# Kernel tuning notes

Measured on AMD Instinct MI355X. Metric: run time of the kernel, lower is better.

Reference implementation:

```python
import jax, jax.numpy as jnp
import numpy as np

BUCKETS = 32
DIM = 1024
HEADS = 16
TEMP = 0.75
SINK_ITERS = 7
LOG_EPS = 1e-6
GUMBEL_EPS = 1e-4


def _sinkhorn(r, n_iters):
    # iterative row/col log-normalization, then exp (matches torch loop)
    for _ in range(n_iters):
        r = r - jax.scipy.special.logsumexp(r, axis=2, keepdims=True)
        r = r - jax.scipy.special.logsumexp(r, axis=1, keepdims=True)
    return jnp.exp(r)


def setup_inputs() -> dict:
    key = jax.random.key(0)
    kq, kk, kv, kw, kg = jax.random.split(key, 5)
    B, H, T, DH = 4, 16, 4096, 64
    q = jax.random.normal(kq, (B, H, T, DH), jnp.float32)
    k = jax.random.normal(kk, (B, H, T, DH), jnp.float32)
    v = jax.random.normal(kv, (B, H, T, DH), jnp.float32)
    sort_w = jax.random.normal(kw, (1, H, DH, BUCKETS), jnp.float32)
    u = jax.random.uniform(kg, (B * H, BUCKETS, BUCKETS), jnp.float32, 0.0, 1.0)
    gumbel_noise = -jnp.log(-jnp.log(u + GUMBEL_EPS) + GUMBEL_EPS)
    return {"q": q, "k": k, "v": v, "sort_w": sort_w, "gumbel_noise": gumbel_noise}


def reference(q, k, v, sort_w, gumbel_noise):
    b, h, t, dh = q.shape
    bh = b * h
    bsz = t // BUCKETS  # tokens per bucket
    # bucket: (bh, buckets, bsz, dh)
    qb = q.reshape(bh, BUCKETS, bsz, dh)
    kb = k.reshape(bh, BUCKETS, bsz, dh)
    vb = v.reshape(bh, BUCKETS, bsz, dh)
    # bucket summaries for routing
    b_k_r = kb.sum(axis=2)  # (bh, buckets, dh)
    e_w = jnp.broadcast_to(sort_w, (b, h, dh, BUCKETS)).reshape(bh, dh, BUCKETS)
    R = jnp.log(jax.nn.relu(jnp.einsum('bud,bdv->buv', b_k_r, e_w)) + LOG_EPS)
    R = (R + gumbel_noise) / TEMP
    R = _sinkhorn(R, SINK_ITERS)  # soft permutation matrix (bh, buckets, buckets)
    R = jnp.tril(R, -1)  # causal: only attend to strictly earlier buckets
    # soft-permute key/value buckets
    k_re = jnp.einsum('buv,bvtd->butd', R, kb)
    v_re = jnp.einsum('buv,bvtd->butd', R, vb)
    bk = jnp.concatenate([k_re, kb], axis=2)  # (bh, buckets, 2*bsz, dh)
    bv = jnp.concatenate([v_re, vb], axis=2)
    dots = jnp.einsum('buie,buje->buij', qb, bk) * (DIM ** -0.5)
    attn = jax.nn.softmax(dots, axis=-1)
    out = jnp.einsum('buij,buje->buie', attn, bv)  # (bh, buckets, bsz, dh)
    return out.reshape(b, h, t, dh)
```

## Files before the change

### kernel.cpp

```cpp
#include <hip/hip_runtime.h>
#include <hip/hip_bf16.h>

#define BUCKETS 32
#define BSZ 128
#define DH 64
#define TEMPINV 1.3333333333333333f
#define SINK_ITERS 7
#define LOG_EPS 1e-6f
#define SCALE 0.03125f

typedef short bf16x8 __attribute__((ext_vector_type(8)));
typedef float f32x4 __attribute__((ext_vector_type(4)));

__device__ __forceinline__ void bf8_to_f32(const uint4 x, float* f) {
    f[0] = __uint_as_float(x.x << 16);
    f[1] = __uint_as_float(x.x & 0xffff0000u);
    f[2] = __uint_as_float(x.y << 16);
    f[3] = __uint_as_float(x.y & 0xffff0000u);
    f[4] = __uint_as_float(x.z << 16);
    f[5] = __uint_as_float(x.z & 0xffff0000u);
    f[6] = __uint_as_float(x.w << 16);
    f[7] = __uint_as_float(x.w & 0xffff0000u);
}

__device__ __forceinline__ unsigned f2bf(float f) {
    unsigned x = __float_as_uint(f);
    return (x + 0x7fffu + ((x >> 16) & 1u)) >> 16;
}

__device__ __forceinline__ uint4 packbf8(const float* f) {
    uint4 r;
    r.x = f2bf(f[0]) | (f2bf(f[1]) << 16);
    r.y = f2bf(f[2]) | (f2bf(f[3]) << 16);
    r.z = f2bf(f[4]) | (f2bf(f[5]) << 16);
    r.w = f2bf(f[6]) | (f2bf(f[7]) << 16);
    return r;
}

__device__ __forceinline__ void load_lds16(const uint4* g, uint4* l) {
    __builtin_amdgcn_global_load_lds(
        (const __attribute__((address_space(1))) unsigned int*)g,
        (__attribute__((address_space(3))) unsigned int*)l, 16, 0, 0);
}

__global__ __launch_bounds__(256) void bksum_kernel(
    const float* __restrict__ kptr, float* __restrict__ bkr)
{
    const int t = blockIdx.x;
    const int tid = threadIdx.x;
    __shared__ float4 part[16][17];
    const float4* k4 = (const float4*)kptr + (size_t)t * 2048;
    const int c4 = tid & 15, rg = tid >> 4;
    float4 s; s.x = 0.f; s.y = 0.f; s.z = 0.f; s.w = 0.f;
    for (int r = rg; r < 128; r += 16) {
        float4 a = k4[r * 16 + c4];
        s.x += a.x; s.y += a.y; s.z += a.z; s.w += a.w;
    }
    part[rg][c4] = s;
    __syncthreads();
    if (tid < 16) {
        float4 acc = part[0][tid];
        for (int g = 1; g < 16; ++g) {
            float4 p = part[g][tid];
            acc.x += p.x; acc.y += p.y; acc.z += p.z; acc.w += p.w;
        }
        ((float4*)bkr)[t * 16 + tid] = acc;
    }
}

__global__ __launch_bounds__(256) void sinkhorn_kernel(
    const float* __restrict__ bkrp,
    const float* __restrict__ swptr,
    const float* __restrict__ gptr,
    float* __restrict__ Rout)
{
    const int b = blockIdx.x;
    const int h = b & 15;
    const int tid = threadIdx.x;

    __shared__ float bk[BUCKETS][DH];
    __shared__ float sw[DH][BUCKETS];
    __shared__ float R[BUCKETS][BUCKETS + 1];

    for (int o = tid; o < DH * BUCKETS; o += 256)
        sw[o >> 5][o & 31] = swptr[h * DH * BUCKETS + o];
    for (int o = tid; o < BUCKETS * DH; o += 256)
        bk[o >> 6][o & 63] = bkrp[b * 2048 + o];
    __syncthreads();

    for (int o = tid; o < BUCKETS * BUCKETS; o += 256) {
        const int uu = o >> 5, vv = o & 31;
        float dot = 0.f;
        for (int d = 0; d < DH; ++d) dot = fmaf(bk[uu][d], sw[d][vv], dot);
        const float g = gptr[b * 1024 + o];
        R[uu][vv] = (logf(fmaxf(dot, 0.f) + LOG_EPS) + g) * TEMPINV;
    }
    __syncthreads();

    for (int it = 0; it < SINK_ITERS; ++it) {
        if (tid < BUCKETS) {
            float m = -1e30f;
            for (int j = 0; j < BUCKETS; ++j) m = fmaxf(m, R[tid][j]);
            float s = 0.f;
            for (int j = 0; j < BUCKETS; ++j) s += expf(R[tid][j] - m);
            const float lse = m + logf(s);
            for (int j = 0; j < BUCKETS; ++j) R[tid][j] -= lse;
        }
        __syncthreads();
        if (tid < BUCKETS) {
            float m = -1e30f;
            for (int j = 0; j < BUCKETS; ++j) m = fmaxf(m, R[j][tid]);
            float s = 0.f;
            for (int j = 0; j < BUCKETS; ++j) s += expf(R[j][tid] - m);
            const float lse = m + logf(s);
            for (int j = 0; j < BUCKETS; ++j) R[j][tid] -= lse;
        }
        __syncthreads();
    }

    for (int o = tid; o < BUCKETS * BUCKETS; o += 256) {
        const int uu = o >> 5, vv = o & 31;
        Rout[b * 1024 + o] = (vv < uu) ? expf(R[uu][vv]) : 0.f;
    }
}

__global__ __launch_bounds__(256) void reshuffle2_kernel(
    const float* __restrict__ kptr,
    const float* __restrict__ vptr,
    const float* __restrict__ Rmat,
    uint4* __restrict__ kimg,
    uint4* __restrict__ vimg)
{
    const int j0 = blockIdx.x;
    const int b  = blockIdx.y;
    const int tid = threadIdx.x;
    const int u = tid >> 3, c8 = tid & 7;

    __shared__ float ls[32][8][64];
    __shared__ float lr[32][33];

    for (int o = tid; o < 1024; o += 256)
        lr[o >> 5][o & 31] = Rmat[b * 1024 + o];

    float4* ls4 = (float4*)ls;

    {
        const float4* kb4 = (const float4*)kptr + (size_t)b * 65536 + j0 * 128;
        for (int it = 0; it < 16; ++it) {
            const int idx = it * 256 + tid;
            const int v = idx >> 7, i = idx & 127;
            ls4[v * 128 + i] = kb4[v * 2048 + i];
        }
    }
    __syncthreads();
    {
        float ka[8][8];
        #pragma unroll
        for (int r = 0; r < 8; ++r)
            #pragma unroll
            for (int t = 0; t < 8; ++t) ka[r][t] = 0.f;
        for (int vv = 0; vv < u; ++vv) {
            const float rw = lr[u][vv];
            #pragma unroll
            for (int r = 0; r < 8; ++r)
                #pragma unroll
                for (int t = 0; t < 8; ++t)
                    ka[r][t] = fmaf(rw, ls[vv][r][c8 * 8 + t], ka[r][t]);
        }
        uint4* kdst = kimg + ((size_t)b * 32 + u) * 2048;
        #pragma unroll
        for (int r = 0; r < 8; ++r) {
            kdst[(j0 * 8 + r) * 8 + (c8 ^ r)] = packbf8(ka[r]);
            float o8[8];
            #pragma unroll
            for (int t = 0; t < 8; ++t) o8[t] = ls[u][r][c8 * 8 + t];
            kdst[(128 + j0 * 8 + r) * 8 + (c8 ^ r)] = packbf8(o8);
        }
    }
    __syncthreads();

    {
        const float4* vb4 = (const float4*)vptr + (size_t)b * 65536 + j0 * 128;
        for (int it = 0; it < 16; ++it) {
            const int idx = it * 256 + tid;
            const int v = idx >> 7, i = idx & 127;
            ls4[v * 128 + i] = vb4[v * 2048 + i];
        }
    }
    __syncthreads();
    {
        float va[8][8];
        #pragma unroll
        for (int r = 0; r < 8; ++r)
            #pragma unroll
            for (int t = 0; t < 8; ++t) va[r][t] = 0.f;
        for (int vv = 0; vv < u; ++vv) {
            const float rw = lr[u][vv];
            #pragma unroll
            for (int r = 0; r < 8; ++r)
                #pragma unroll
                for (int t = 0; t < 8; ++t)
                    va[r][t] = fmaf(rw, ls[vv][r][c8 * 8 + t], va[r][t]);
        }
        uint4* vdst = vimg + ((size_t)b * 32 + u) * 2048;
        #pragma unroll
        for (int t = 0; t < 8; ++t) {
            const int blk = c8 * 8 + (t ^ c8);
            uint4 wre;
            wre.x = f2bf(va[0][t]) | (f2bf(va[1][t]) << 16);
            wre.y = f2bf(va[2][t]) | (f2bf(va[3][t]) << 16);
            wre.z = f2bf(va[4][t]) | (f2bf(va[5][t]) << 16);
            wre.w = f2bf(va[6][t]) | (f2bf(va[7][t]) << 16);
            vdst[j0 * 64 + blk] = wre;
            uint4 wor;
            wor.x = f2bf(ls[u][0][c8 * 8 + t]) | (f2bf(ls[u][1][c8 * 8 + t]) << 16);
            wor.y = f2bf(ls[u][2][c8 * 8 + t]) | (f2bf(ls[u][3][c8 * 8 + t]) << 16);
            wor.z = f2bf(ls[u][4][c8 * 8 + t]) | (f2bf(ls[u][5][c8 * 8 + t]) << 16);
            wor.w = f2bf(ls[u][6][c8 * 8 + t]) | (f2bf(ls[u][7][c8 * 8 + t]) << 16);
            vdst[(16 + j0) * 64 + blk] = wor;
        }
    }
}

__global__ __launch_bounds__(128) void attn_fallback(
    const float* __restrict__ qptr,
    const float* __restrict__ kptr,
    const float* __restrict__ vptr,
    const float* __restrict__ Rmat,
    float4* __restrict__ optr)
{
    const int u = blockIdx.x;
    const int b = blockIdx.y;
    const int tid = threadIdx.x;

    __shared__ uint4 sbk[2048];
    __shared__ uint4 sbv[2048];

    const float4* k4 = (const float4*)kptr + (size_t)b * 65536;
    const float4* v4 = (const float4*)vptr + (size_t)b * 65536;
    const float4* q4 = (const float4*)qptr + (size_t)b * 65536;

    const float* Rrow = Rmat + (b * BUCKETS + u) * BUCKETS;
    for (int o = tid; o < 1024; o += 128) {
        float ka[8] = {0.f,0.f,0.f,0.f,0.f,0.f,0.f,0.f};
        float va[8] = {0.f,0.f,0.f,0.f,0.f,0.f,0.f,0.f};
        for (int vv = 0; vv < u; ++vv) {
            const float r = Rrow[vv];
            float4 a = k4[vv * 2048 + 2 * o], c = k4[vv * 2048 + 2 * o + 1];
            ka[0] = fmaf(r, a.x, ka[0]); ka[1] = fmaf(r, a.y, ka[1]);
            ka[2] = fmaf(r, a.z, ka[2]); ka[3] = fmaf(r, a.w, ka[3]);
            ka[4] = fmaf(r, c.x, ka[4]); ka[5] = fmaf(r, c.y, ka[5]);
            ka[6] = fmaf(r, c.z, ka[6]); ka[7] = fmaf(r, c.w, ka[7]);
            float4 av = v4[vv * 2048 + 2 * o], cv = v4[vv * 2048 + 2 * o + 1];
            va[0] = fmaf(r, av.x, va[0]); va[1] = fmaf(r, av.y, va[1]);
            va[2] = fmaf(r, av.z, va[2]); va[3] = fmaf(r, av.w, va[3]);
            va[4] = fmaf(r, cv.x, va[4]); va[5] = fmaf(r, cv.y, va[5]);
            va[6] = fmaf(r, cv.z, va[6]); va[7] = fmaf(r, cv.w, va[7]);
        }
        sbk[o] = packbf8(ka);
        sbv[o] = packbf8(va);
        float4 a = k4[u * 2048 + 2 * o], c = k4[u * 2048 + 2 * o + 1];
        float f[8] = {a.x,a.y,a.z,a.w,c.x,c.y,c.z,c.w};
        sbk[1024 + o] = packbf8(f);
        float4 av = v4[u * 2048 + 2 * o], cv = v4[u * 2048 + 2 * o + 1];
        float g[8] = {av.x,av.y,av.z,av.w,cv.x,cv.y,cv.z,cv.w};
        sbv[1024 + o] = packbf8(g);
    }
    __syncthreads();

    const int i = tid;
    float qr[64];
    const float4* qrow = q4 + (u * 128 + i) * 16;
    for (int d4 = 0; d4 < 16; ++d4) {
        float4 t = qrow[d4];
        qr[d4 * 4 + 0] = t.x; qr[d4 * 4 + 1] = t.y;
        qr[d4 * 4 + 2] = t.z; qr[d4 * 4 + 3] = t.w;
    }

    float acc[64];
    for (int d = 0; d < 64; ++d) acc[d] = 0.f;
    float l = 0.f;

    for (int j = 0; j < 256; ++j) {
        float s = 0.f;
        for (int d8 = 0; d8 < 8; ++d8) {
            float f[8];
            bf8_to_f32(sbk[j * 8 + d8], f);
            for (int t = 0; t < 8; ++t) s = fmaf(qr[d8 * 8 + t], f[t], s);
        }
        const float p = __expf(s * SCALE);
        l += p;
        for (int d8 = 0; d8 < 8; ++d8) {
            float f[8];
            bf8_to_f32(sbv[j * 8 + d8], f);
            for (int t = 0; t < 8; ++t)
                acc[d8 * 8 + t] = fmaf(p, f[t], acc[d8 * 8 + t]);
        }
    }

    const float inv = 1.f / l;
    float4* orow = optr + (size_t)b * 65536 + (u * 128 + i) * 16;
    for (int d4 = 0; d4 < 16; ++d4) {
        float4 t;
        t.x = acc[d4 * 4 + 0] * inv;
        t.y = acc[d4 * 4 + 1] * inv;
        t.z = acc[d4 * 4 + 2] * inv;
        t.w = acc[d4 * 4 + 3] * inv;
        orow[d4] = t;
    }
}

__global__ __launch_bounds__(256) void attn_mfma2(
    const float* __restrict__ qptr,
    const uint4* __restrict__ kimg,
    const uint4* __restrict__ vimg,
    float* __restrict__ optr)
{
    const int u = blockIdx.x;
    const int b = blockIdx.y;
    const int tid = threadIdx.x;
    const int lane = tid & 63;
    const int w = tid >> 6;
    const int lg = lane >> 4;
    const int lr = lane & 15;

    __shared__ uint4 sK[2048];
    __shared__ uint4 sV[2048];
    __shared__ uint4 sP[1024];

    const size_t tile = (size_t)b * 32 + u;
    const uint4* gk = kimg + tile * 2048;
    const uint4* gv = vimg + tile * 2048;

    #pragma unroll
    for (int it = 0; it < 8; ++it)
        load_lds16(gk + it * 256 + tid, &sK[it * 256 + (w << 6)]);
    #pragma unroll
    for (int it = 0; it < 8; ++it)
        load_lds16(gv + it * 256 + tid, &sV[it * 256 + (w << 6)]);

    const float* qbase = qptr + (size_t)b * 262144 + (size_t)u * 8192;
    bf16x8 qf[2][2];
    #pragma unroll
    for (int mt = 0; mt < 2; ++mt)
        #pragma unroll
        for (int c = 0; c < 2; ++c) {
            const int row = w * 32 + mt * 16 + lr;
            const float4* qr = (const float4*)(qbase + row * 64 + (c * 4 + lg) * 8);
            float4 a = qr[0], cc = qr[1];
            float f[8] = {a.x * SCALE, a.y * SCALE, a.z * SCALE, a.w * SCALE,
                          cc.x * SCALE, cc.y * SCALE, cc.z * SCALE, cc.w * SCALE};
            uint4 tq = packbf8(f);
            qf[mt][c] = *(bf16x8*)&tq;
        }
    __syncthreads();

    uint4* sPw = sP + w * 256;
    unsigned short* sPh = (unsigned short*)sPw;

    f32x4 acc[2][4];
    float lsum[2][4];
    #pragma unroll
    for (int mt = 0; mt < 2; ++mt) {
        #pragma unroll
        for (int nt = 0; nt < 4; ++nt) {
            acc[mt][nt][0] = 0.f; acc[mt][nt][1] = 0.f;
            acc[mt][nt][2] = 0.f; acc[mt][nt][3] = 0.f;
        }
        #pragma unroll
        for (int r = 0; r < 4; ++r) lsum[mt][r] = 0.f;
    }

    for (int kb = 0; kb < 4; ++kb) {
        bf16x8 kf[4][2];
        #pragma unroll
        for (int nt = 0; nt < 4; ++nt)
            #pragma unroll
            for (int c = 0; c < 2; ++c) {
                const int j = kb * 64 + nt * 16 + lr;
                const int dcu = c * 4 + lg;
                uint4 t = sK[j * 8 + (dcu ^ (j & 7))];
                kf[nt][c] = *(bf16x8*)&t;
            }
        f32x4 s[2][4];
        #pragma unroll
        for (int mt = 0; mt < 2; ++mt)
            #pragma unroll
            for (int nt = 0; nt < 4; ++nt) {
                s[mt][nt][0] = 0.f; s[mt][nt][1] = 0.f;
                s[mt][nt][2] = 0.f; s[mt][nt][3] = 0.f;
            }
        __builtin_amdgcn_s_setprio(1);
        #pragma unroll
        for (int c = 0; c < 2; ++c)
            #pragma unroll
            for (int mt = 0; mt < 2; ++mt)
                #pragma unroll
                for (int nt = 0; nt < 4; ++nt)
                    s[mt][nt] = __builtin_amdgcn_mfma_f32_16x16x32_bf16(
                        qf[mt][c], kf[nt][c], s[mt][nt], 0, 0, 0);
        __builtin_amdgcn_s_setprio(0);

        #pragma unroll
        for (int mt = 0; mt < 2; ++mt)
            #pragma unroll
            for (int nt = 0; nt < 4; ++nt)
                #pragma unroll
                for (int r = 0; r < 4; ++r) {
                    const float p = __expf(s[mt][nt][r]);
                    lsum[mt][r] += p;
                    const int row = mt * 16 + lg * 4 + r;
                    const int col = nt * 16 + lr;
                    sPh[row * 64 + (((col >> 3) ^ (row & 7)) << 3) + (col & 7)] =
                        (unsigned short)f2bf(p);
                }
        asm volatile("s_waitcnt lgkmcnt(0)" ::: "memory");
        __builtin_amdgcn_sched_barrier(0);

        bf16x8 pf[2][2];
        #pragma unroll
        for (int mt = 0; mt < 2; ++mt)
            #pragma unroll
            for (int c = 0; c < 2; ++c) {
                const int row = mt * 16 + lr;
                const int dcu = c * 4 + lg;
                uint4 t = sPw[row * 8 + (dcu ^ (row & 7))];
                pf[mt][c] = *(bf16x8*)&t;
            }
        bf16x8 vf[4][2];
        #pragma unroll
        for (int nt = 0; nt < 4; ++nt)
            #pragma unroll
            for (int c = 0; c < 2; ++c) {
                const int p = kb * 8 + c * 4 + lg;
                const int d = nt * 16 + lr;
                const int blk = (d >> 3) * 8 + ((d & 7) ^ ((d >> 3) & 7));
                uint4 t = sV[p * 64 + blk];
                vf[nt][c] = *(bf16x8*)&t;
            }
        __builtin_amdgcn_s_setprio(1);
        #pragma unroll
        for (int c = 0; c < 2; ++c)
            #pragma unroll
            for (int mt = 0; mt < 2; ++mt)
                #pragma unroll
                for (int nt = 0; nt < 4; ++nt)
                    acc[mt][nt] = __builtin_amdgcn_mfma_f32_16x16x32_bf16(
                        pf[mt][c], vf[nt][c], acc[mt][nt], 0, 0, 0);
        __builtin_amdgcn_s_setprio(0);
    }

    #pragma unroll
    for (int mt = 0; mt < 2; ++mt)
        #pragma unroll
        for (int r = 0; r < 4; ++r) {
            float sum = lsum[mt][r];
            sum += __shfl_xor(sum, 1);
            sum += __shfl_xor(sum, 2);
            sum += __shfl_xor(sum, 4);
            sum += __shfl_xor(sum, 8);
            const float inv = 1.f / sum;
            const int row = mt * 16 + lg * 4 + r;
            float* orow = optr + (size_t)b * 262144 +
                          (size_t)(u * 128 + w * 32 + row) * 64;
            #pragma unroll
            for (int nt = 0; nt < 4; ++nt)
                orow[nt * 16 + lr] = acc[mt][nt][r] * inv;
        }
}

extern "C" void kernel_launch(void* const* d_in, const int* in_sizes, int n_in,
                              void* d_out, int out_size, void* d_ws, size_t ws_size,
                              hipStream_t stream) {
    const float* q  = (const float*)d_in[0];
    const float* k  = (const float*)d_in[1];
    const float* v  = (const float*)d_in[2];
    const float* sw = (const float*)d_in[3];
    const float* g  = (const float*)d_in[4];

    float* R    = (float*)d_ws;
    float* bkr  = (float*)((char*)d_ws + 262144);
    uint4* kimg = (uint4*)((char*)d_ws + 1048576);
    uint4* vimg = (uint4*)((char*)d_ws + 1048576 + 67108864);
    const bool big_ws = (ws_size >= (size_t)1048576 + 2u * 67108864u);

    bksum_kernel<<<dim3(2048), dim3(256), 0, stream>>>(k, bkr);
    sinkhorn_kernel<<<dim3(64), dim3(256), 0, stream>>>(bkr, sw, g, R);
    if (big_ws) {
        reshuffle2_kernel<<<dim3(16, 64), dim3(256), 0, stream>>>(k, v, R, kimg, vimg);
        attn_mfma2<<<dim3(32, 64), dim3(256), 0, stream>>>(q, kimg, vimg, (float*)d_out);
    } else {
        attn_fallback<<<dim3(32, 64), dim3(128), 0, stream>>>(q, k, v, R, (float4*)d_out);
    }
}
```

Baseline: 328.8 us.

## Fuse sinkhorn into reshuffle kernel, parallelize LSE, halve reshuffle tile

Drops the separate sinkhorn launch on the main path: each reshuffle block now recomputes the routing logits and runs the Sinkhorn normalization itself, and the row and column logsumexp uses 256 threads with shuffle reductions instead of 32 serial threads. Each reshuffle block now handles 4 token rows instead of 8, doubling the grid to 32x64 and halving shared memory, with launch bounds set for higher occupancy. The cost is that the routing and Sinkhorn work is repeated 32 times per head-batch, and V writes become 8-byte half stores.

Result: slower. 340.4 us (+3.5%).

```diff
diff --git a/kernel.cpp b/kernel.cpp
--- a/kernel.cpp
+++ b/kernel.cpp
@@ -97,25 +97,36 @@
     }
     __syncthreads();
 
+    const int rr = tid >> 3, sub = tid & 7;
     for (int it = 0; it < SINK_ITERS; ++it) {
-        if (tid < BUCKETS) {
-            float m = -1e30f;
-            for (int j = 0; j < BUCKETS; ++j) m = fmaxf(m, R[tid][j]);
-            float s = 0.f;
-            for (int j = 0; j < BUCKETS; ++j) s += expf(R[tid][j] - m);
+        {
+            float vals[4];
+            float m = -1e30f, s = 0.f;
+            #pragma unroll
+            for (int q = 0; q < 4; ++q) { vals[q] = R[rr][sub * 4 + q]; m = fmaxf(m, vals[q]); }
+            m = fmaxf(m, __shfl_xor(m, 1)); m = fmaxf(m, __shfl_xor(m, 2)); m = fmaxf(m, __shfl_xor(m, 4));
+            #pragma unroll
+            for (int q = 0; q < 4; ++q) s += expf(vals[q] - m);
+            s += __shfl_xor(s, 1); s += __shfl_xor(s, 2); s += __shfl_xor(s, 4);
             const float lse = m + logf(s);
-            for (int j = 0; j < BUCKETS; ++j) R[tid][j] -= lse;
-        }
-        __syncthreads();
-        if (tid < BUCKETS) {
-            float m = -1e30f;
-            for (int j = 0; j < BUCKETS; ++j) m = fmaxf(m, R[j][tid]);
-            float s = 0.f;
-            for (int j = 0; j < BUCKETS; ++j) s += expf(R[j][tid] - m);
+            #pragma unroll
+            for (int q = 0; q < 4; ++q) R[rr][sub * 4 + q] = vals[q] - lse;
+            __syncthreads();
+        }
+        {
+            float vals[4];
+            float m = -1e30f, s = 0.f;
+            #pragma unroll
+            for (int q = 0; q < 4; ++q) { vals[q] = R[sub * 4 + q][rr]; m = fmaxf(m, vals[q]); }
+            m = fmaxf(m, __shfl_xor(m, 1)); m = fmaxf(m, __shfl_xor(m, 2)); m = fmaxf(m, __shfl_xor(m, 4));
+            #pragma unroll
+            for (int q = 0; q < 4; ++q) s += expf(vals[q] - m);
+            s += __shfl_xor(s, 1); s += __shfl_xor(s, 2); s += __shfl_xor(s, 4);
             const float lse = m + logf(s);
-            for (int j = 0; j < BUCKETS; ++j) R[j][tid] -= lse;
-        }
-        __syncthreads();
+            #pragma unroll
+            for (int q = 0; q < 4; ++q) R[sub * 4 + q][rr] = vals[q] - lse;
+            __syncthreads();
+        }
     }
 
     for (int o = tid; o < BUCKETS * BUCKETS; o += 256) {
@@ -124,100 +135,150 @@
     }
 }
 
-__global__ __launch_bounds__(256) void reshuffle2_kernel(
+__global__ __launch_bounds__(256, 4) void reshuffle3_kernel(
     const float* __restrict__ kptr,
     const float* __restrict__ vptr,
-    const float* __restrict__ Rmat,
+    const float* __restrict__ bkrp,
+    const float* __restrict__ swptr,
+    const float* __restrict__ gptr,
     uint4* __restrict__ kimg,
     uint4* __restrict__ vimg)
 {
     const int j0 = blockIdx.x;
     const int b  = blockIdx.y;
+    const int h  = b & 15;
     const int tid = threadIdx.x;
     const int u = tid >> 3, c8 = tid & 7;
 
-    __shared__ float ls[32][8][64];
+    __shared__ float ls[32][4][64];
     __shared__ float lr[32][33];
 
-    for (int o = tid; o < 1024; o += 256)
-        lr[o >> 5][o & 31] = Rmat[b * 1024 + o];
+    float* bk  = &ls[0][0][0];
+    float* swl = bk + 2048;
+
+    for (int o = tid; o < 2048; o += 256) bk[o]  = bkrp[b * 2048 + o];
+    for (int o = tid; o < 2048; o += 256) swl[o] = swptr[h * 2048 + o];
+    __syncthreads();
+    for (int o = tid; o < 1024; o += 256) {
+        const int uu = o >> 5, vv = o & 31;
+        float dot = 0.f;
+        for (int d = 0; d < 64; ++d) dot = fmaf(bk[uu * 64 + d], swl[d * 32 + vv], dot);
+        lr[uu][vv] = (logf(fmaxf(dot, 0.f) + LOG_EPS) + gptr[b * 1024 + o]) * TEMPINV;
+    }
+    __syncthreads();
+
+    const int rr = tid >> 3, sub = tid & 7;
+    for (int it = 0; it < SINK_ITERS; ++it) {
+        {
+            float vals[4];
+            float m = -1e30f, s = 0.f;
+            #pragma unroll
+            for (int q = 0; q < 4; ++q) { vals[q] = lr[rr][sub * 4 + q]; m = fmaxf(m, vals[q]); }
+            m = fmaxf(m, __shfl_xor(m, 1)); m = fmaxf(m, __shfl_xor(m, 2)); m = fmaxf(m, __shfl_xor(m, 4));
+            #pragma unroll
+            for (int q = 0; q < 4; ++q) s += expf(vals[q] - m);
+            s += __shfl_xor(s, 1); s += __shfl_xor(s, 2); s += __shfl_xor(s, 4);
+            const float lse = m + logf(s);
+            #pragma unroll
+            for (int q = 0; q < 4; ++q) lr[rr][sub * 4 + q] = vals[q] - lse;
+            __syncthreads();
+        }
+        {
+            float vals[4];
+            float m = -1e30f, s = 0.f;
+            #pragma unroll
+            for (int q = 0; q < 4; ++q) { vals[q] = lr[sub * 4 + q][rr]; m = fmaxf(m, vals[q]); }
+            m = fmaxf(m, __shfl_xor(m, 1)); m = fmaxf(m, __shfl_xor(m, 2)); m = fmaxf(m, __shfl_xor(m, 4));
+            #pragma unroll
+            for (int q = 0; q < 4; ++q) s += expf(vals[q] - m);
+            s += __shfl_xor(s, 1); s += __shfl_xor(s, 2); s += __shfl_xor(s, 4);
+            const float lse = m + logf(s);
+            #pragma unroll
+            for (int q = 0; q < 4; ++q) lr[sub * 4 + q][rr] = vals[q] - lse;
+            __syncthreads();
+        }
+    }
+    for (int o = tid; o < 1024; o += 256) {
+        const int uu = o >> 5, vv = o & 31;
+        const float val = lr[uu][vv];
+        lr[uu][vv] = (vv < uu) ? expf(val) : 0.f;
+    }
+    __syncthreads();
 
     float4* ls4 = (float4*)ls;
 
     {
-        const float4* kb4 = (const float4*)kptr + (size_t)b * 65536 + j0 * 128;
-        for (int it = 0; it < 16; ++it) {
+        const float4* kb4 = (const float4*)kptr + (size_t)b * 65536 + j0 * 64;
+        for (int it = 0; it < 8; ++it) {
             const int idx = it * 256 + tid;
-            const int v = idx >> 7, i = idx & 127;
-            ls4[v * 128 + i] = kb4[v * 2048 + i];
+            const int v = idx >> 6, i = idx & 63;
+            ls4[v * 64 + i] = kb4[v * 2048 + i];
         }
     }
     __syncthreads();
     {
-        float ka[8][8];
-        #pragma unroll
-        for (int r = 0; r < 8; ++r)
+        float ka[4][8];
+        #pragma unroll
+        for (int r = 0; r < 4; ++r)
             #pragma unroll
             for (int t = 0; t < 8; ++t) ka[r][t] = 0.f;
         for (int vv = 0; vv < u; ++vv) {
-            const float rw = lr[u][vv];
-            #pragma unroll
-            for (int r = 0; r < 8; ++r)
+            const float rwt = lr[u][vv];
+            #pragma unroll
+            for (int r = 0; r < 4; ++r)
                 #pragma unroll
                 for (int t = 0; t < 8; ++t)
-                    ka[r][t] = fmaf(rw, ls[vv][r][c8 * 8 + t], ka[r][t]);
+                    ka[r][t] = fmaf(rwt, ls[vv][r][c8 * 8 + t], ka[r][t]);
         }
         uint4* kdst = kimg + ((size_t)b * 32 + u) * 2048;
         #pragma unroll
-        for (int r = 0; r < 8; ++r) {
-            kdst[(j0 * 8 + r) * 8 + (c8 ^ r)] = packbf8(ka[r]);
+        for (int r = 0; r < 4; ++r) {
+            const int j = j0 * 4 + r;
+            kdst[j * 8 + (c8 ^ (j & 7))] = packbf8(ka[r]);
             float o8[8];
             #pragma unroll
             for (int t = 0; t < 8; ++t) o8[t] = ls[u][r][c8 * 8 + t];
-            kdst[(128 + j0 * 8 + r) * 8 + (c8 ^ r)] = packbf8(o8);
+            kdst[(128 + j) * 8 + (c8 ^ (j & 7))] = packbf8(o8);
         }
     }
     __syncthreads();
 
     {
-        const float4* vb4 = (const float4*)vptr + (size_t)b * 65536 + j0 * 128;
-        for (int it = 0; it < 16; ++it) {
+        const float4* vb4 = (const float4*)vptr + (size_t)b * 65536 + j0 * 64;
+        for (int it = 0; it < 8; ++it) {
             const int idx = it * 256 + tid;
-            const int v = idx >> 7, i = idx & 127;
-            ls4[v * 128 + i] = vb4[v * 2048 + i];
+            const int v = idx >> 6, i = idx & 63;
+            ls4[v * 64 + i] = vb4[v * 2048 + i];
         }
     }
     __syncthreads();
     {
-        float va[8][8];
-        #pragma unroll
-        for (int r = 0; r < 8; ++r)
+        float va[4][8];
+        #pragma unroll
+        for (int r = 0; r < 4; ++r)
             #pragma unroll
             for (int t = 0; t < 8; ++t) va[r][t] = 0.f;
         for (int vv = 0; vv < u; ++vv) {
-            const float rw = lr[u][vv];
-            #pragma unroll
-            for (int r = 0; r < 8; ++r)
+            const float rwt = lr[u][vv];
+            #pragma unroll
+            for (int r = 0; r < 4; ++r)
                 #pragma unroll
                 for (int t = 0; t < 8; ++t)
-                    va[r][t] = fmaf(rw, ls[vv][r][c8 * 8 + t], va[r][t]);
-        }
-        uint4* vdst = vimg + ((size_t)b * 32 + u) * 2048;
+                    va[r][t] = fmaf(rwt, ls[vv][r][c8 * 8 + t], va[r][t]);
+        }
+        uint2* vdst2 = (uint2*)(vimg + ((size_t)b * 32 + u) * 2048);
+        const int p = j0 >> 1, half = j0 & 1;
         #pragma unroll
         for (int t = 0; t < 8; ++t) {
             const int blk = c8 * 8 + (t ^ c8);
-            uint4 wre;
+            uint2 wre;
             wre.x = f2bf(va[0][t]) | (f2bf(va[1][t]) << 16);
             wre.y = f2bf(va[2][t]) | (f2bf(va[3][t]) << 16);
-            wre.z = f2bf(va[4][t]) | (f2bf(va[5][t]) << 16);
-            wre.w = f2bf(va[6][t]) | (f2bf(va[7][t]) << 16);
-            vdst[j0 * 64 + blk] = wre;
-            uint4 wor;
+            vdst2[(p * 64 + blk) * 2 + half] = wre;
+            uint2 wor;
             wor.x = f2bf(ls[u][0][c8 * 8 + t]) | (f2bf(ls[u][1][c8 * 8 + t]) << 16);
             wor.y = f2bf(ls[u][2][c8 * 8 + t]) | (f2bf(ls[u][3][c8 * 8 + t]) << 16);
-            wor.z = f2bf(ls[u][4][c8 * 8 + t]) | (f2bf(ls[u][5][c8 * 8 + t]) << 16);
-            wor.w = f2bf(ls[u][6][c8 * 8 + t]) | (f2bf(ls[u][7][c8 * 8 + t]) << 16);
-            vdst[(16 + j0) * 64 + blk] = wor;
+            vdst2[((16 + p) * 64 + blk) * 2 + half] = wor;
         }
     }
 }
@@ -485,11 +546,11 @@
     const bool big_ws = (ws_size >= (size_t)1048576 + 2u * 67108864u);
 
     bksum_kernel<<<dim3(2048), dim3(256), 0, stream>>>(k, bkr);
-    sinkhorn_kernel<<<dim3(64), dim3(256), 0, stream>>>(bkr, sw, g, R);
     if (big_ws) {
-        reshuffle2_kernel<<<dim3(16, 64), dim3(256), 0, stream>>>(k, v, R, kimg, vimg);
+        reshuffle3_kernel<<<dim3(32, 64), dim3(256), 0, stream>>>(k, v, bkr, sw, g, kimg, vimg);
         attn_mfma2<<<dim3(32, 64), dim3(256), 0, stream>>>(q, kimg, vimg, (float*)d_out);
     } else {
+        sinkhorn_kernel<<<dim3(64), dim3(256), 0, stream>>>(bkr, sw, g, R);
         attn_fallback<<<dim3(32, 64), dim3(128), 0, stream>>>(q, k, v, R, (float4*)d_out);
     }
 }
```
